# Kernel optimization log

Hardware: AMD Instinct MI355X
Metric: run time of the kernel (lower is better)

Reference implementation:

```python
import jax, jax.numpy as jnp
import numpy as np

NUM_HEADS = 8
DIM = 256  # == out_dim; module implicitly requires dim == out_dim


def setup_inputs() -> dict:
    key = jax.random.key(0)
    k0, k1, k2, k3, k4, k5 = jax.random.split(key, 6)
    B, N, T, dim = 4, 128, 128, DIM
    s = dim ** -0.5
    return {
        "v": jax.random.normal(k0, (B, N, T, dim), dtype=jnp.float32),
        "Wq": jax.random.normal(k1, (dim, dim), dtype=jnp.float32) * s,
        "Wk": jax.random.normal(k2, (dim, dim), dtype=jnp.float32) * s,
        "Wv": jax.random.normal(k3, (dim, dim), dtype=jnp.float32) * s,
        "Wp": jax.random.normal(k4, (dim, dim), dtype=jnp.float32) * s,
        "bp": jax.random.normal(k5, (dim,), dtype=jnp.float32) * 0.01,
    }


def reference(v, Wq, Wk, Wv, Wp, bp):
    B, N, T, dim = v.shape
    H = NUM_HEADS
    hd = dim // H
    scale = hd ** -0.5
    # projections (qkv_bias=False)
    q = (v @ Wq).reshape(B * N, T, H, hd)
    k = (v @ Wk).reshape(B * N, T, H, hd)
    vv = (v @ Wv).reshape(B * N, T, H, hd)
    # NOTE: heads axis is NOT moved before the matmul in the original torch
    # code, so attention is over the HEADS axis: per (b*n, t) an HxH matrix.
    attn = jnp.einsum('mthd,mtgd->mthg', q, k) * scale  # [B*N, T, H, H]
    attn = jax.nn.softmax(attn, axis=-1)
    x = jnp.einsum('mthg,mtgd->mthd', attn, vv).reshape(B, N, T, dim)
    # output projection (with bias); dropout probs are 0 / eval mode
    return x @ Wp + bp
```

## Files before the change

kernel.cpp:

```cpp
#include <hip/hip_runtime.h>
#include <hip/hip_bf16.h>
#include <math.h>


#define DIMX      256
#define NH        8
#define HD        32
#define TM        64
#define NTHREADS  1024
#define QSTRIDE   776
#define KT        8
#define NT_QKV    48

typedef _Float16 f16x8 __attribute__((ext_vector_type(8)));
typedef _Float16 f16x4 __attribute__((ext_vector_type(4)));
typedef _Float16 f16x2 __attribute__((ext_vector_type(2)));
typedef float    f32x4 __attribute__((ext_vector_type(4)));

static __device__ __forceinline__ f16x2 pkrtz(float a, float b) {
    return (f16x2)__builtin_amdgcn_cvt_pkrtz(a, b);
}

__global__ void pack_weights(const float* __restrict__ Wq,
                             const float* __restrict__ Wk,
                             const float* __restrict__ Wv,
                             const float* __restrict__ Wp,
                             _Float16* __restrict__ pk)
{
    const int QKV_FRAGS = NT_QKV * KT * 64;
    int u = blockIdx.x * blockDim.x + threadIdx.x;
    const float* W;
    int nt, kt, lane;
    if (u < QKV_FRAGS) {
        nt = u / (KT * 64); kt = (u / 64) % KT; lane = u % 64;
        if (nt < 16)      { W = Wq; }
        else if (nt < 32) { W = Wk; nt -= 16; }
        else              { W = Wv; nt -= 32; }
    } else {
        int u2 = u - QKV_FRAGS;
        nt = u2 / (KT * 64); kt = (u2 / 64) % KT; lane = u2 % 64;
        W = Wp;
    }
    const int n  = nt * 16 + (lane & 15);
    const int k0 = kt * 32 + (lane >> 4) * 8;
    f16x8 frag;
#pragma unroll
    for (int j = 0; j < 8; ++j)
        frag[j] = (_Float16)W[(size_t)(k0 + j) * DIMX + n];
    *(f16x8*)(pk + (size_t)u * 8) = frag;
}

__global__ __launch_bounds__(NTHREADS, 4)
void fused_attn_mfma(const float* __restrict__ v,
                     const _Float16* __restrict__ Wqkv_pk,
                     const _Float16* __restrict__ Wp_pk,
                     const float* __restrict__ bp,
                     float* __restrict__ out)
{
    __shared__ __align__(16) _Float16 S[TM * QSTRIDE];

    const int tid   = threadIdx.x;
    const int lane  = tid & 63;
    const int wv_id = tid >> 6;
    const int l15   = lane & 15;
    const int quad  = lane >> 4;
    const long token0 = (long)blockIdx.x * TM;

    const int tiles[3] = { 16 + 2 * wv_id, 17 + 2 * wv_id, wv_id };

    const float4* src = (const float4*)(v + token0 * DIMX);
    float4 t4[4];
#pragma unroll
    for (int i = 0; i < 4; ++i)
        t4[i] = src[tid + NTHREADS * i];

    const f16x8* wb  = (const f16x8*)Wqkv_pk + lane;
    const f16x8* wb2 = (const f16x8*)Wp_pk + lane;
    f16x8 Wr[8];
#pragma unroll
    for (int p = 0; p < 8; ++p)
        Wr[p] = wb[(size_t)(tiles[p % 3] * KT + p / 3) * 64];

#pragma unroll
    for (int i = 0; i < 4; ++i) {
        int u = tid + NTHREADS * i;
        int m = u >> 6;
        int c = (u & 63) * 4;
        f16x2 lo = pkrtz(t4[i].x, t4[i].y), hi = pkrtz(t4[i].z, t4[i].w);
        f16x4 b4 = { lo.x, lo.y, hi.x, hi.y };
        *(f16x4*)&S[m * QSTRIDE + c] = b4;
    }
    __syncthreads();

    f32x4 acc[3][4];
#pragma unroll
    for (int jj = 0; jj < 3; ++jj)
#pragma unroll
        for (int tt = 0; tt < 4; ++tt)
            acc[jj][tt] = (f32x4){0.f, 0.f, 0.f, 0.f};

#pragma unroll
    for (int kt = 0; kt < KT; ++kt) {
        f16x8 vf[4];
#pragma unroll
        for (int tt = 0; tt < 4; ++tt)
            vf[tt] = *(const f16x8*)&S[(tt * 16 + l15) * QSTRIDE + kt * 32 + quad * 8];
#pragma unroll
        for (int jj = 0; jj < 3; ++jj) {
            const int u = kt * 3 + jj;
            f16x8 w = Wr[u & 7];
            const int un = u + 8;
            if (un < 24)
                Wr[u & 7] = wb[(size_t)(tiles[un % 3] * KT + un / 3) * 64];
            else
                Wr[u & 7] = wb2[(size_t)(wv_id * KT + (un - 24)) * 64];
#pragma unroll
            for (int tt = 0; tt < 4; ++tt)
                acc[jj][tt] = __builtin_amdgcn_mfma_f32_16x16x32_f16(w, vf[tt], acc[jj][tt], 0, 0, 0);
        }
    }

#pragma unroll
    for (int jj = 0; jj < 2; ++jj)
#pragma unroll
        for (int tt = 0; tt < 4; ++tt) {
            f16x2 a = pkrtz(acc[jj][tt][0], acc[jj][tt][1]);
            f16x2 b = pkrtz(acc[jj][tt][2], acc[jj][tt][3]);
            f16x4 p4 = { a.x, a.y, b.x, b.y };
            *(f16x4*)&S[(tt * 16 + l15) * QSTRIDE + tiles[jj] * 16 + quad * 4] = p4;
        }
    __syncthreads();

#pragma unroll
    for (int tt = 0; tt < 4; ++tt) {
        f16x2 a = pkrtz(acc[2][tt][0], acc[2][tt][1]);
        f16x2 b = pkrtz(acc[2][tt][2], acc[2][tt][3]);
        f16x4 p4 = { a.x, a.y, b.x, b.y };
        *(f16x4*)&S[(tt * 16 + l15) * QSTRIDE + tiles[2] * 16 + quad * 4] = p4;
    }
    __syncthreads();

    {
        const int ta  = tid >> 4;
        const int sub = tid & 15;
        const int h   = sub >> 1;
        const int d0  = (sub & 1) * 16;
        const float scale = 0.17677669529663687f;

        const _Float16* qrow  = &S[ta * QSTRIDE + h * HD + d0];
        const _Float16* kbase = &S[ta * QSTRIDE + 256 + d0];
        const _Float16* vbase = &S[ta * QSTRIDE + 512 + d0];

        f16x8 q0 = *(const f16x8*)qrow;
        f16x8 q1 = *(const f16x8*)(qrow + 8);

        float logits[NH];
#pragma unroll
        for (int g = 0; g < NH; ++g) {
            f16x8 k0 = *(const f16x8*)(kbase + g * HD);
            f16x8 k1 = *(const f16x8*)(kbase + g * HD + 8);
            f16x8 p  = q0 * k0;
            p += q1 * k1;
            f16x4 r4 = __builtin_shufflevector(p, p, 0, 1, 2, 3)
                     + __builtin_shufflevector(p, p, 4, 5, 6, 7);
            f16x2 r2 = __builtin_shufflevector(r4, r4, 0, 1)
                     + __builtin_shufflevector(r4, r4, 2, 3);
            logits[g] = (float)r2.x + (float)r2.y;
        }
#pragma unroll
        for (int g = 0; g < NH; ++g)
            logits[g] = (logits[g] + __shfl_xor(logits[g], 1, 64)) * scale;

        float mx = logits[0];
#pragma unroll
        for (int g = 1; g < NH; ++g) mx = fmaxf(mx, logits[g]);
        float se = 0.f;
#pragma unroll
        for (int g = 0; g < NH; ++g) { logits[g] = __expf(logits[g] - mx); se += logits[g]; }
        float inv = 1.f / se;

        f16x8 xa0 = (f16x8)(_Float16)0.f;
        f16x8 xa1 = (f16x8)(_Float16)0.f;
#pragma unroll
        for (int g = 0; g < NH; ++g) {
            _Float16 ph = (_Float16)(logits[g] * inv);
            f16x8 pw = { ph, ph, ph, ph, ph, ph, ph, ph };
            f16x8 v0 = *(const f16x8*)(vbase + g * HD);
            f16x8 v1 = *(const f16x8*)(vbase + g * HD + 8);
            xa0 += pw * v0;
            xa1 += pw * v1;
        }
        __syncthreads();
        *(f16x8*)&S[ta * QSTRIDE + h * HD + d0]     = xa0;
        *(f16x8*)&S[ta * QSTRIDE + h * HD + d0 + 8] = xa1;
    }
    __syncthreads();

    {
        f32x4 acc2[4];
#pragma unroll
        for (int tt = 0; tt < 4; ++tt)
            acc2[tt] = (f32x4){0.f, 0.f, 0.f, 0.f};

#pragma unroll
        for (int kt = 0; kt < KT; ++kt) {
            f16x8 xf[4];
#pragma unroll
            for (int tt = 0; tt < 4; ++tt)
                xf[tt] = *(const f16x8*)&S[(tt * 16 + l15) * QSTRIDE + kt * 32 + quad * 8];
            f16x8 w = Wr[kt];
#pragma unroll
            for (int tt = 0; tt < 4; ++tt)
                acc2[tt] = __builtin_amdgcn_mfma_f32_16x16x32_f16(w, xf[tt], acc2[tt], 0, 0, 0);
        }

        f32x4 b = *(const f32x4*)&bp[wv_id * 16 + quad * 4];
#pragma unroll
        for (int tt = 0; tt < 4; ++tt) {
            f32x4 o = acc2[tt] + b;
            *(f32x4*)&out[(token0 + tt * 16 + l15) * DIMX + wv_id * 16 + quad * 4] = o;
        }
    }
}

extern "C" void kernel_launch(void* const* d_in, const int* in_sizes, int n_in,
                              void* d_out, int out_size, void* d_ws, size_t ws_size,
                              hipStream_t stream) {
    const float* v  = (const float*)d_in[0];
    const float* Wq = (const float*)d_in[1];
    const float* Wk = (const float*)d_in[2];
    const float* Wv = (const float*)d_in[3];
    const float* Wp = (const float*)d_in[4];
    const float* bp = (const float*)d_in[5];
    float* out = (float*)d_out;

    _Float16* pk = (_Float16*)d_ws;
    const _Float16* Wqkv_pk = pk;
    const _Float16* Wp_pk   = pk + (size_t)24576 * 8;

    pack_weights<<<256, 128, 0, stream>>>(Wq, Wk, Wv, Wp, pk);

    const int ntokens = in_sizes[0] / DIMX;
    fused_attn_mfma<<<ntokens / TM, NTHREADS, 0, stream>>>(v, Wqkv_pk, Wp_pk, bp, out);
}
```

Baseline: 171.1 us.

## Loop each block over four token tiles and prefetch the next input tile

Each block now processes four consecutive 64-token tiles in a loop, so the grid shrinks by four. The next tile's input is loaded from global memory during the attention phase and written to a separate LDS region (column 512 onward). QKV tiles are reassigned so each wave computes three adjacent tiles. The output projection is re-split into a 2x2 per-wave tiling, and its weights stream through a 4-register ring. This amortises the setup and weight-fragment loads and overlaps the input fetch with compute, at the cost of fewer blocks in flight (256 instead of 1024) and more register pressure.

After: 273.1 us. +59.6%, slower.

```diff
diff --git a/kernel.cpp b/kernel.cpp
--- a/kernel.cpp
+++ b/kernel.cpp
@@ -7,6 +7,7 @@
 #define NH        8
 #define HD        32
 #define TM        64
+#define GITER     4
 #define NTHREADS  1024
 #define QSTRIDE   776
 #define KT        8
@@ -64,161 +65,199 @@
     const int wv_id = tid >> 6;
     const int l15   = lane & 15;
     const int quad  = lane >> 4;
-    const long token0 = (long)blockIdx.x * TM;
-
-    const int tiles[3] = { 16 + 2 * wv_id, 17 + 2 * wv_id, wv_id };
-
-    const float4* src = (const float4*)(v + token0 * DIMX);
-    float4 t4[4];
-#pragma unroll
-    for (int i = 0; i < 4; ++i)
-        t4[i] = src[tid + NTHREADS * i];
-
-    const f16x8* wb  = (const f16x8*)Wqkv_pk + lane;
-    const f16x8* wb2 = (const f16x8*)Wp_pk + lane;
+    const int t3    = 3 * wv_id;
+    const int i2    = wv_id >> 1;
+    const int jj    = wv_id & 1;
+
+    const long blk0 = (long)blockIdx.x * (GITER * TM);
+
+    const f16x8* wbA = (const f16x8*)Wqkv_pk + lane;
+    const f16x8* wbB = (const f16x8*)Wp_pk + lane;
     f16x8 Wr[8];
-#pragma unroll
-    for (int p = 0; p < 8; ++p)
-        Wr[p] = wb[(size_t)(tiles[p % 3] * KT + p / 3) * 64];
-
-#pragma unroll
-    for (int i = 0; i < 4; ++i) {
-        int u = tid + NTHREADS * i;
-        int m = u >> 6;
-        int c = (u & 63) * 4;
-        f16x2 lo = pkrtz(t4[i].x, t4[i].y), hi = pkrtz(t4[i].z, t4[i].w);
-        f16x4 b4 = { lo.x, lo.y, hi.x, hi.y };
-        *(f16x4*)&S[m * QSTRIDE + c] = b4;
+    f16x8 W2[4];
+
+    {
+        const float4* src = (const float4*)(v + blk0 * DIMX);
+        float4 t4[4];
+#pragma unroll
+        for (int i = 0; i < 4; ++i)
+            t4[i] = src[tid + NTHREADS * i];
+#pragma unroll
+        for (int p = 0; p < 8; ++p)
+            Wr[p] = wbA[(size_t)((t3 + p % 3) * KT + p / 3) * 64];
+#pragma unroll
+        for (int i = 0; i < 4; ++i) {
+            int u = tid + NTHREADS * i;
+            int m = u >> 6;
+            int c = (u & 63) * 4;
+            f16x2 lo = pkrtz(t4[i].x, t4[i].y), hi = pkrtz(t4[i].z, t4[i].w);
+            f16x4 b4 = { lo.x, lo.y, hi.x, hi.y };
+            *(f16x4*)&S[m * QSTRIDE + 512 + c] = b4;
+        }
+        __syncthreads();
     }
-    __syncthreads();
-
-    f32x4 acc[3][4];
-#pragma unroll
-    for (int jj = 0; jj < 3; ++jj)
-#pragma unroll
-        for (int tt = 0; tt < 4; ++tt)
-            acc[jj][tt] = (f32x4){0.f, 0.f, 0.f, 0.f};
-
-#pragma unroll
-    for (int kt = 0; kt < KT; ++kt) {
-        f16x8 vf[4];
-#pragma unroll
-        for (int tt = 0; tt < 4; ++tt)
-            vf[tt] = *(const f16x8*)&S[(tt * 16 + l15) * QSTRIDE + kt * 32 + quad * 8];
-#pragma unroll
-        for (int jj = 0; jj < 3; ++jj) {
-            const int u = kt * 3 + jj;
-            f16x8 w = Wr[u & 7];
-            const int un = u + 8;
-            if (un < 24)
-                Wr[u & 7] = wb[(size_t)(tiles[un % 3] * KT + un / 3) * 64];
-            else
-                Wr[u & 7] = wb2[(size_t)(wv_id * KT + (un - 24)) * 64];
+
+#pragma unroll 1
+    for (int g = 0; g < GITER; ++g) {
+        const long token0 = blk0 + (long)g * TM;
+
+        f32x4 acc[3][4];
+#pragma unroll
+        for (int j = 0; j < 3; ++j)
 #pragma unroll
             for (int tt = 0; tt < 4; ++tt)
-                acc[jj][tt] = __builtin_amdgcn_mfma_f32_16x16x32_f16(w, vf[tt], acc[jj][tt], 0, 0, 0);
-        }
-    }
-
-#pragma unroll
-    for (int jj = 0; jj < 2; ++jj)
-#pragma unroll
-        for (int tt = 0; tt < 4; ++tt) {
-            f16x2 a = pkrtz(acc[jj][tt][0], acc[jj][tt][1]);
-            f16x2 b = pkrtz(acc[jj][tt][2], acc[jj][tt][3]);
-            f16x4 p4 = { a.x, a.y, b.x, b.y };
-            *(f16x4*)&S[(tt * 16 + l15) * QSTRIDE + tiles[jj] * 16 + quad * 4] = p4;
-        }
-    __syncthreads();
-
-#pragma unroll
-    for (int tt = 0; tt < 4; ++tt) {
-        f16x2 a = pkrtz(acc[2][tt][0], acc[2][tt][1]);
-        f16x2 b = pkrtz(acc[2][tt][2], acc[2][tt][3]);
-        f16x4 p4 = { a.x, a.y, b.x, b.y };
-        *(f16x4*)&S[(tt * 16 + l15) * QSTRIDE + tiles[2] * 16 + quad * 4] = p4;
-    }
-    __syncthreads();
-
-    {
-        const int ta  = tid >> 4;
-        const int sub = tid & 15;
-        const int h   = sub >> 1;
-        const int d0  = (sub & 1) * 16;
-        const float scale = 0.17677669529663687f;
-
-        const _Float16* qrow  = &S[ta * QSTRIDE + h * HD + d0];
-        const _Float16* kbase = &S[ta * QSTRIDE + 256 + d0];
-        const _Float16* vbase = &S[ta * QSTRIDE + 512 + d0];
-
-        f16x8 q0 = *(const f16x8*)qrow;
-        f16x8 q1 = *(const f16x8*)(qrow + 8);
-
-        float logits[NH];
-#pragma unroll
-        for (int g = 0; g < NH; ++g) {
-            f16x8 k0 = *(const f16x8*)(kbase + g * HD);
-            f16x8 k1 = *(const f16x8*)(kbase + g * HD + 8);
-            f16x8 p  = q0 * k0;
-            p += q1 * k1;
-            f16x4 r4 = __builtin_shufflevector(p, p, 0, 1, 2, 3)
-                     + __builtin_shufflevector(p, p, 4, 5, 6, 7);
-            f16x2 r2 = __builtin_shufflevector(r4, r4, 0, 1)
-                     + __builtin_shufflevector(r4, r4, 2, 3);
-            logits[g] = (float)r2.x + (float)r2.y;
-        }
-#pragma unroll
-        for (int g = 0; g < NH; ++g)
-            logits[g] = (logits[g] + __shfl_xor(logits[g], 1, 64)) * scale;
-
-        float mx = logits[0];
-#pragma unroll
-        for (int g = 1; g < NH; ++g) mx = fmaxf(mx, logits[g]);
-        float se = 0.f;
-#pragma unroll
-        for (int g = 0; g < NH; ++g) { logits[g] = __expf(logits[g] - mx); se += logits[g]; }
-        float inv = 1.f / se;
-
-        f16x8 xa0 = (f16x8)(_Float16)0.f;
-        f16x8 xa1 = (f16x8)(_Float16)0.f;
-#pragma unroll
-        for (int g = 0; g < NH; ++g) {
-            _Float16 ph = (_Float16)(logits[g] * inv);
-            f16x8 pw = { ph, ph, ph, ph, ph, ph, ph, ph };
-            f16x8 v0 = *(const f16x8*)(vbase + g * HD);
-            f16x8 v1 = *(const f16x8*)(vbase + g * HD + 8);
-            xa0 += pw * v0;
-            xa1 += pw * v1;
-        }
-        __syncthreads();
-        *(f16x8*)&S[ta * QSTRIDE + h * HD + d0]     = xa0;
-        *(f16x8*)&S[ta * QSTRIDE + h * HD + d0 + 8] = xa1;
-    }
-    __syncthreads();
-
-    {
-        f32x4 acc2[4];
-#pragma unroll
-        for (int tt = 0; tt < 4; ++tt)
-            acc2[tt] = (f32x4){0.f, 0.f, 0.f, 0.f};
+                acc[j][tt] = (f32x4){0.f, 0.f, 0.f, 0.f};
 
 #pragma unroll
         for (int kt = 0; kt < KT; ++kt) {
-            f16x8 xf[4];
+            f16x8 vf[4];
 #pragma unroll
             for (int tt = 0; tt < 4; ++tt)
-                xf[tt] = *(const f16x8*)&S[(tt * 16 + l15) * QSTRIDE + kt * 32 + quad * 8];
-            f16x8 w = Wr[kt];
-#pragma unroll
-            for (int tt = 0; tt < 4; ++tt)
-                acc2[tt] = __builtin_amdgcn_mfma_f32_16x16x32_f16(w, xf[tt], acc2[tt], 0, 0, 0);
-        }
-
-        f32x4 b = *(const f32x4*)&bp[wv_id * 16 + quad * 4];
-#pragma unroll
-        for (int tt = 0; tt < 4; ++tt) {
-            f32x4 o = acc2[tt] + b;
-            *(f32x4*)&out[(token0 + tt * 16 + l15) * DIMX + wv_id * 16 + quad * 4] = o;
+                vf[tt] = *(const f16x8*)&S[(tt * 16 + l15) * QSTRIDE + 512 + kt * 32 + quad * 8];
+#pragma unroll
+            for (int j = 0; j < 3; ++j) {
+                const int u = kt * 3 + j;
+                f16x8 w = Wr[u & 7];
+                if (u + 8 < 24) {
+                    const int un = u + 8;
+                    Wr[u & 7] = wbA[(size_t)((t3 + un % 3) * KT + un / 3) * 64];
+                }
+#pragma unroll
+                for (int tt = 0; tt < 4; ++tt)
+                    acc[j][tt] = __builtin_amdgcn_mfma_f32_16x16x32_f16(w, vf[tt], acc[j][tt], 0, 0, 0);
+            }
+        }
+        __syncthreads();
+
+#pragma unroll
+        for (int j = 0; j < 3; ++j)
+#pragma unroll
+            for (int tt = 0; tt < 4; ++tt) {
+                f16x2 a = pkrtz(acc[j][tt][0], acc[j][tt][1]);
+                f16x2 b = pkrtz(acc[j][tt][2], acc[j][tt][3]);
+                f16x4 p4 = { a.x, a.y, b.x, b.y };
+                *(f16x4*)&S[(tt * 16 + l15) * QSTRIDE + (t3 + j) * 16 + quad * 4] = p4;
+            }
+        __syncthreads();
+
+        float4 t4[4];
+        if (g + 1 < GITER) {
+            const float4* srcn = (const float4*)(v + (token0 + TM) * DIMX);
+#pragma unroll
+            for (int i = 0; i < 4; ++i)
+                t4[i] = srcn[tid + NTHREADS * i];
+        }
+#pragma unroll
+        for (int p = 0; p < 4; ++p)
+            W2[p] = wbB[(size_t)((2 * i2 + (p & 1)) * KT + (p >> 1)) * 64];
+
+        {
+            const int ta  = tid >> 4;
+            const int sub = tid & 15;
+            const int h   = sub >> 1;
+            const int d0  = (sub & 1) * 16;
+            const float scale = 0.17677669529663687f;
+
+            const _Float16* qrow  = &S[ta * QSTRIDE + h * HD + d0];
+            const _Float16* kbase = &S[ta * QSTRIDE + 256 + d0];
+            const _Float16* vbase = &S[ta * QSTRIDE + 512 + d0];
+
+            f16x8 q0 = *(const f16x8*)qrow;
+            f16x8 q1 = *(const f16x8*)(qrow + 8);
+
+            float logits[NH];
+#pragma unroll
+            for (int g2 = 0; g2 < NH; ++g2) {
+                f16x8 k0 = *(const f16x8*)(kbase + g2 * HD);
+                f16x8 k1 = *(const f16x8*)(kbase + g2 * HD + 8);
+                f16x8 p  = q0 * k0;
+                p += q1 * k1;
+                f16x4 r4 = __builtin_shufflevector(p, p, 0, 1, 2, 3)
+                         + __builtin_shufflevector(p, p, 4, 5, 6, 7);
+                f16x2 r2 = __builtin_shufflevector(r4, r4, 0, 1)
+                         + __builtin_shufflevector(r4, r4, 2, 3);
+                logits[g2] = (float)r2.x + (float)r2.y;
+            }
+#pragma unroll
+            for (int g2 = 0; g2 < NH; ++g2)
+                logits[g2] = (logits[g2] + __shfl_xor(logits[g2], 1, 64)) * scale;
+
+            float mx = logits[0];
+#pragma unroll
+            for (int g2 = 1; g2 < NH; ++g2) mx = fmaxf(mx, logits[g2]);
+            float se = 0.f;
+#pragma unroll
+            for (int g2 = 0; g2 < NH; ++g2) { logits[g2] = __expf(logits[g2] - mx); se += logits[g2]; }
+            float inv = 1.f / se;
+
+            f16x8 xa0 = (f16x8)(_Float16)0.f;
+            f16x8 xa1 = (f16x8)(_Float16)0.f;
+#pragma unroll
+            for (int g2 = 0; g2 < NH; ++g2) {
+                _Float16 ph = (_Float16)(logits[g2] * inv);
+                f16x8 pw = { ph, ph, ph, ph, ph, ph, ph, ph };
+                f16x8 v0 = *(const f16x8*)(vbase + g2 * HD);
+                f16x8 v1 = *(const f16x8*)(vbase + g2 * HD + 8);
+                xa0 += pw * v0;
+                xa1 += pw * v1;
+            }
+            __syncthreads();
+            *(f16x8*)&S[ta * QSTRIDE + h * HD + d0]     = xa0;
+            *(f16x8*)&S[ta * QSTRIDE + h * HD + d0 + 8] = xa1;
+        }
+
+        if (g + 1 < GITER) {
+#pragma unroll
+            for (int i = 0; i < 4; ++i) {
+                int u = tid + NTHREADS * i;
+                int m = u >> 6;
+                int c = (u & 63) * 4;
+                f16x2 lo = pkrtz(t4[i].x, t4[i].y), hi = pkrtz(t4[i].z, t4[i].w);
+                f16x4 b4v = { lo.x, lo.y, hi.x, hi.y };
+                *(f16x4*)&S[m * QSTRIDE + 512 + c] = b4v;
+            }
+        }
+        __syncthreads();
+
+        {
+            f32x4 acc2[2][2];
+#pragma unroll
+            for (int jx = 0; jx < 2; ++jx)
+#pragma unroll
+                for (int tt = 0; tt < 2; ++tt)
+                    acc2[jx][tt] = (f32x4){0.f, 0.f, 0.f, 0.f};
+
+#pragma unroll
+            for (int kt = 0; kt < KT; ++kt) {
+                f16x8 xf[2];
+#pragma unroll
+                for (int tt = 0; tt < 2; ++tt)
+                    xf[tt] = *(const f16x8*)&S[(jj * 32 + tt * 16 + l15) * QSTRIDE + kt * 32 + quad * 8];
+#pragma unroll
+                for (int jx = 0; jx < 2; ++jx) {
+                    const int u2 = kt * 2 + jx;
+                    f16x8 w = W2[u2 & 3];
+                    if (u2 + 4 < 16)
+                        W2[u2 & 3] = wbB[(size_t)((2 * i2 + jx) * KT + (kt + 2)) * 64];
+                    acc2[jx][0] = __builtin_amdgcn_mfma_f32_16x16x32_f16(w, xf[0], acc2[jx][0], 0, 0, 0);
+                    acc2[jx][1] = __builtin_amdgcn_mfma_f32_16x16x32_f16(w, xf[1], acc2[jx][1], 0, 0, 0);
+                }
+                if (kt == 4 && g + 1 < GITER) {
+#pragma unroll
+                    for (int p = 0; p < 8; ++p)
+                        Wr[p] = wbA[(size_t)((t3 + p % 3) * KT + p / 3) * 64];
+                }
+            }
+
+#pragma unroll
+            for (int jx = 0; jx < 2; ++jx) {
+                f32x4 b = *(const f32x4*)&bp[(2 * i2 + jx) * 16 + quad * 4];
+#pragma unroll
+                for (int tt = 0; tt < 2; ++tt) {
+                    f32x4 o = acc2[jx][tt] + b;
+                    *(f32x4*)&out[(token0 + jj * 32 + tt * 16 + l15) * DIMX + (2 * i2 + jx) * 16 + quad * 4] = o;
+                }
+            }
         }
     }
 }
@@ -241,5 +280,5 @@
     pack_weights<<<256, 128, 0, stream>>>(Wq, Wk, Wv, Wp, pk);
 
     const int ntokens = in_sizes[0] / DIMX;
-    fused_attn_mfma<<<ntokens / TM, NTHREADS, 0, stream>>>(v, Wqkv_pk, Wp_pk, bp, out);
-}
+    fused_attn_mfma<<<ntokens / (TM * GITER), NTHREADS, 0, stream>>>(v, Wqkv_pk, Wp_pk, bp, out);
+}
```
